# Kernel optimization log

Measured on AMD Instinct MI355X. Metric: run time of the kernel, lower is better.

The kernel has to match this reference:

```python
import jax, jax.numpy as jnp
import numpy as np
import math

NUM_HEADS = 16
D_MODEL = 1024
BATCH = 1
SEQ_LEN = 4096


def alibi_slopes(num_heads):
    # slopes m_h = (256 ** (1/H)) ** -(h+1)
    x = (2.0 ** 8) ** (1.0 / num_heads)
    return jnp.asarray([1.0 / x ** (i + 1) for i in range(num_heads)], dtype=jnp.float32)


def setup_inputs() -> dict:
    key = jax.random.key(0)
    k1, k2 = jax.random.split(key)
    x = jax.random.normal(k1, (BATCH, SEQ_LEN, D_MODEL), dtype=jnp.float32)
    # nn.Linear(d_model, 3*d_model, bias=False); store as [d_model, 3*d_model] so y = x @ w
    w_kqv = jax.random.normal(k2, (D_MODEL, 3 * D_MODEL), dtype=jnp.float32) * (1.0 / math.sqrt(D_MODEL))
    return {"x": x, "w_kqv": w_kqv}


def reference(x, w_kqv):
    B, S, D = x.shape
    H = NUM_HEADS
    dh = D // H
    scale = jnp.asarray(math.sqrt(D), dtype=x.dtype)  # module divides by sqrt(d_model)

    kqv = x @ w_kqv  # [B, S, 3D]
    # NOTE: original chunks as (key, query, value) in that order
    k, q, v = jnp.split(kqv, 3, axis=-1)
    q = q.reshape(B, S, H, dh)
    k = k.reshape(B, S, H, dh)
    v = v.reshape(B, S, H, dh)

    # ALiBi bias: m_h * (j - i), shape [H, S, S]
    pos = jnp.arange(S)
    rel = pos[None, :] - pos[:, None]  # [S, S], x - y
    slopes = alibi_slopes(H).astype(x.dtype)  # [H]
    bias = slopes[:, None, None] * rel.astype(x.dtype)  # [H, S, S]

    score = jnp.einsum('bihd,bjhd->bhij', q, k) / scale + bias[None]  # [B, H, S, S]
    causal = rel <= 0  # j <= i (lower triangular)
    score = jnp.where(causal[None, None], score, jnp.asarray(-jnp.inf, dtype=score.dtype))

    attn = jax.nn.softmax(score, axis=-1)
    out = jnp.einsum('bhij,bjhd->bihd', attn, v).reshape(B, S, D)
    return out
```

## Files before the change

kernel.cpp:

```cpp
#include <hip/hip_runtime.h>
#include <stdint.h>
#include <math.h>

#define SEQ 4096
#define DM  1024
#define NH  16
#define DH  64
#define LOG2E 1.44269504088896341f

typedef short bf16x8 __attribute__((ext_vector_type(8)));
typedef short bf16x4 __attribute__((ext_vector_type(4)));
typedef float f32x4  __attribute__((ext_vector_type(4)));
typedef uint32_t u32x4 __attribute__((ext_vector_type(4)));

typedef const __attribute__((address_space(1))) short* gptr_t;
typedef __attribute__((address_space(3))) short* lptr_t;

__device__ __forceinline__ short f2bf(float f) {
    union { float f; uint32_t u; } x; x.f = f;
    uint32_t r = (x.u + 0x7fffu + ((x.u >> 16) & 1u)) >> 16;
    return (short)r;
}
__device__ __forceinline__ short f2bf_trunc(float f) {
    union { float f; uint32_t u; } x; x.f = f;
    return (short)(x.u >> 16);
}
__device__ __forceinline__ uint32_t pkbf(float lo, float hi) {
    union { float f; uint32_t u; } a, b; a.f = lo; b.f = hi;
    return (a.u >> 16) | (b.u & 0xffff0000u);
}

__device__ __forceinline__ void load_lds16(const short* g, const short* l) {
    __builtin_amdgcn_global_load_lds((gptr_t)(uintptr_t)g,
                                     (lptr_t)(uint32_t)(uintptr_t)l, 16, 0, 0);
}

__global__ __launch_bounds__(256) void cvt_fused(const float* __restrict__ x,
                                                 const float* __restrict__ w,
                                                 short* __restrict__ xb,
                                                 short* __restrict__ wtb) {
    __shared__ float T[64][69];
    const int b = blockIdx.x;
    if (b < 2048) {
        const int i = (b * 256 + threadIdx.x) * 8;
        float4 a0 = ((const float4*)(x + i))[0];
        float4 a1 = ((const float4*)(x + i))[1];
        bf16x8 p;
        p[0]=f2bf(a0.x); p[1]=f2bf(a0.y); p[2]=f2bf(a0.z); p[3]=f2bf(a0.w);
        p[4]=f2bf(a1.x); p[5]=f2bf(a1.y); p[6]=f2bf(a1.z); p[7]=f2bf(a1.w);
        *(bf16x8*)(xb + i) = p;
        return;
    }
    const int bb = b - 2048;
    const int n0 = (bb % 48) * 64, k0 = (bb / 48) * 64;
    const int t = threadIdx.x;
    {
        const int kr = t >> 4, nc = (t & 15) * 4;
        #pragma unroll
        for (int i = 0; i < 4; ++i) {
            float4 v = *(const float4*)(w + (size_t)(k0 + kr + i * 16) * 3072 + n0 + nc);
            T[kr + i * 16][nc + 0] = v.x; T[kr + i * 16][nc + 1] = v.y;
            T[kr + i * 16][nc + 2] = v.z; T[kr + i * 16][nc + 3] = v.w;
        }
    }
    __syncthreads();
    const int nr = t >> 4, kc = (t & 15) * 4;
    #pragma unroll
    for (int i = 0; i < 4; ++i) {
        const int n = n0 + nr + i * 16;
        const float sc = (n >= 1024 && n < 2048) ? (LOG2E / 32.0f) : 1.0f;
        short4 o;
        o.x = f2bf(T[kc + 0][nr + i * 16] * sc);
        o.y = f2bf(T[kc + 1][nr + i * 16] * sc);
        o.z = f2bf(T[kc + 2][nr + i * 16] * sc);
        o.w = f2bf(T[kc + 3][nr + i * 16] * sc);
        *(short4*)(wtb + (size_t)n * 1024 + k0 + kc) = o;
    }
}

__global__ __launch_bounds__(256) void qkv_gemm(const short* __restrict__ xb,
                                                const short* __restrict__ wtb,
                                                short* __restrict__ kq,
                                                short* __restrict__ vt) {
    __shared__ short As[128 * 64];
    __shared__ short Bs[128 * 64];
    const int col0 = blockIdx.y * 128, row0 = blockIdx.x * 128;
    const int tid = threadIdx.x, w = tid >> 6, lane = tid & 63;
    const int lmod = lane & 15, ldiv = lane >> 4;
    const int wr = (w >> 1) * 64, wc = (w & 1) * 64;

    f32x4 acc[4][4] = {};
    const short* Ag = xb  + (size_t)row0 * DM;
    const short* Bg = wtb + (size_t)col0 * DM;

    for (int k0 = 0; k0 < DM; k0 += 64) {
        __syncthreads();
        #pragma unroll
        for (int t = 0; t < 4; ++t) {
            const int o = (w * 4 + t) * 1024 + lane * 16;
            const int r = o >> 7, cs = (o & 127) >> 1;
            load_lds16(Ag + (size_t)r * DM + k0 + cs, As + (w * 4 + t) * 512);
            load_lds16(Bg + (size_t)r * DM + k0 + cs, Bs + (w * 4 + t) * 512);
        }
        __syncthreads();
        #pragma unroll
        for (int ks = 0; ks < 2; ++ks) {
            bf16x8 af[4], bf[4];
            #pragma unroll
            for (int i = 0; i < 4; ++i)
                af[i] = *(const bf16x8*)(As + (wr + i * 16 + lmod) * 64 + ks * 32 + ldiv * 8);
            #pragma unroll
            for (int j = 0; j < 4; ++j)
                bf[j] = *(const bf16x8*)(Bs + (wc + j * 16 + lmod) * 64 + ks * 32 + ldiv * 8);
            #pragma unroll
            for (int i = 0; i < 4; ++i)
                #pragma unroll
                for (int j = 0; j < 4; ++j)
                    acc[i][j] = __builtin_amdgcn_mfma_f32_16x16x32_bf16(af[i], bf[j], acc[i][j], 0, 0, 0);
        }
    }

    if (col0 < 2048) {
        #pragma unroll
        for (int i = 0; i < 4; ++i)
            #pragma unroll
            for (int j = 0; j < 4; ++j)
                #pragma unroll
                for (int r = 0; r < 4; ++r)
                    kq[(size_t)(row0 + wr + i * 16 + ldiv * 4 + r) * 2048
                       + col0 + wc + j * 16 + lmod] = f2bf(acc[i][j][r]);
    } else {
        #pragma unroll
        for (int i = 0; i < 4; ++i) {
            const int ig = row0 + wr + i * 16 + ldiv * 4;
            const int kk = ig & 63;
            const int kkp = (kk & 32) | ((kk & 12) << 1) | ((kk & 16) >> 2);
            const int igp = (ig & ~63) | kkp;
            #pragma unroll
            for (int j = 0; j < 4; ++j) {
                const int cg = col0 + wc + j * 16 + lmod - 2048;
                const int h = cg >> 6, d = cg & 63;
                bf16x4 p;
                p[0]=f2bf(acc[i][j][0]); p[1]=f2bf(acc[i][j][1]);
                p[2]=f2bf(acc[i][j][2]); p[3]=f2bf(acc[i][j][3]);
                *(bf16x4*)(vt + (size_t)(h * 64 + d) * SEQ + igp) = p;
            }
        }
    }
}

__global__ __launch_bounds__(256, 4) void attn(const short* __restrict__ kq,
                                               const short* __restrict__ vt,
                                               float* __restrict__ o0,
                                               float* __restrict__ o1,
                                               float* __restrict__ ls0,
                                               float* __restrict__ ls1) {
    __shared__ short Ks[64 * 64];
    __shared__ short Vs[64 * 64];

    const int b = blockIdx.x;
    const int band = b >> 8, pos = b & 255, g = pos >> 5;
    const int qt = (band & 1) ? (24 - band * 8 + g) : (31 - band * 8 - g);
    const int h = (pos >> 1) & 15, s = pos & 1;

    const int tid = threadIdx.x, w = tid >> 6, lane = tid & 63;
    const int lmod = lane & 15, ldiv = lane >> 4;
    const float slope2 = exp2f(-0.5f * (float)(h + 1)) * LOG2E;

    const int sr0 = w * 16 + (lane >> 3), sr1 = sr0 + 8;
    const int sc0 = (lane & 7) ^ (sr0 & 7), sc1 = (lane & 7) ^ (sr1 & 7);

    const int xorm = lmod & 7;
    const int cxs0 = (ldiv ^ xorm) * 8;
    const int cxs1 = ((4 + ldiv) ^ xorm) * 8;

    const int rowbase = qt * 128 + w * 32;

    bf16x8 qf[2][2];
    #pragma unroll
    for (int m = 0; m < 2; ++m) {
        const short* qp = kq + (size_t)(rowbase + m * 16 + lmod) * 2048 + 1024 + h * 64;
        qf[m][0] = *(const bf16x8*)(qp + ldiv * 8);
        qf[m][1] = *(const bf16x8*)(qp + 32 + ldiv * 8);
    }
    int db2[2];
    float pre[2][4];
    #pragma unroll
    for (int m = 0; m < 2; ++m) {
        db2[m] = 4 * ldiv - (rowbase + m * 16 + lmod);
        #pragma unroll
        for (int r = 0; r < 4; ++r) pre[m][r] = slope2 * (float)(db2[m] + r);
    }

    f32x4 O[2][4] = {};
    float lsum[2] = {};
    const int kt0 = s ? (qt + 1) : 0;
    const int kt1 = s ? (2 * qt + 2) : (qt + 1);

    for (int kt = kt0; kt < kt1; ++kt) {
        __syncthreads();
        {
            const short* kb = kq + (size_t)(kt * 64) * 2048 + h * 64;
            load_lds16(kb + (size_t)sr0 * 2048 + sc0 * 8, Ks + (w * 16) * 64);
            load_lds16(kb + (size_t)sr1 * 2048 + sc1 * 8, Ks + (w * 16 + 8) * 64);
            const short* vb = vt + (size_t)(h * 64) * SEQ + kt * 64;
            load_lds16(vb + (size_t)sr0 * SEQ + sc0 * 8, Vs + (w * 16) * 64);
            load_lds16(vb + (size_t)sr1 * SEQ + sc1 * 8, Vs + (w * 16 + 8) * 64);
        }
        __syncthreads();

        const bool diag = (kt >= 2 * qt);
        const int dt = kt * 64;
        const float cb = slope2 * (float)dt;

        #pragma unroll
        for (int ks = 0; ks < 2; ++ks) {
            u32x4 pk0, pk1;
            #pragma unroll
            for (int j1 = 0; j1 < 2; ++j1) {
                const int nt = ks * 2 + j1;
                const float cn = cb + slope2 * (float)(nt * 16);
                f32x4 s0, s1;
                #pragma unroll
                for (int r = 0; r < 4; ++r) { s0[r] = pre[0][r] + cn; s1[r] = pre[1][r] + cn; }
                const short* krow = Ks + (nt * 16 + lmod) * 64;
                const bf16x8 kf0 = *(const bf16x8*)(krow + cxs0);
                const bf16x8 kf1 = *(const bf16x8*)(krow + cxs1);
                s0 = __builtin_amdgcn_mfma_f32_16x16x32_bf16(kf0, qf[0][0], s0, 0, 0, 0);
                s0 = __builtin_amdgcn_mfma_f32_16x16x32_bf16(kf1, qf[0][1], s0, 0, 0, 0);
                s1 = __builtin_amdgcn_mfma_f32_16x16x32_bf16(kf0, qf[1][0], s1, 0, 0, 0);
                s1 = __builtin_amdgcn_mfma_f32_16x16x32_bf16(kf1, qf[1][1], s1, 0, 0, 0);

                float p0[4], p1[4];
                if (diag) {
                    #pragma unroll
                    for (int r = 0; r < 4; ++r) {
                        float v0 = s0[r], v1 = s1[r];
                        if (dt + nt * 16 + r + db2[0] > 0) v0 = -1e30f;
                        if (dt + nt * 16 + r + db2[1] > 0) v1 = -1e30f;
                        p0[r] = __builtin_amdgcn_exp2f(v0);
                        p1[r] = __builtin_amdgcn_exp2f(v1);
                    }
                } else {
                    #pragma unroll
                    for (int r = 0; r < 4; ++r) {
                        p0[r] = __builtin_amdgcn_exp2f(s0[r]);
                        p1[r] = __builtin_amdgcn_exp2f(s1[r]);
                    }
                }
                lsum[0] += (p0[0] + p0[1]) + (p0[2] + p0[3]);
                lsum[1] += (p1[0] + p1[1]) + (p1[2] + p1[3]);
                pk0[j1 * 2]     = pkbf(p0[0], p0[1]);
                pk0[j1 * 2 + 1] = pkbf(p0[2], p0[3]);
                pk1[j1 * 2]     = pkbf(p1[0], p1[1]);
                pk1[j1 * 2 + 1] = pkbf(p1[2], p1[3]);
            }
            const bf16x8 pa0 = __builtin_bit_cast(bf16x8, pk0);
            const bf16x8 pa1 = __builtin_bit_cast(bf16x8, pk1);
            const int cxo = ks ? cxs1 : cxs0;
            #pragma unroll
            for (int nt2 = 0; nt2 < 4; ++nt2) {
                const bf16x8 vf = *(const bf16x8*)(Vs + (nt2 * 16 + lmod) * 64 + cxo);
                O[0][nt2] = __builtin_amdgcn_mfma_f32_16x16x32_bf16(pa0, vf, O[0][nt2], 0, 0, 0);
                O[1][nt2] = __builtin_amdgcn_mfma_f32_16x16x32_bf16(pa1, vf, O[1][nt2], 0, 0, 0);
            }
        }
    }

    #pragma unroll
    for (int m = 0; m < 2; ++m) {
        float v = lsum[m];
        v += __shfl_xor(v, 16);
        v += __shfl_xor(v, 32);
        lsum[m] = v;
    }

    float* ob = s ? o1 : o0;
    float* lb = s ? ls1 : ls0;
    #pragma unroll
    for (int m = 0; m < 2; ++m) {
        const int i0 = rowbase + m * 16 + ldiv * 4;
        #pragma unroll
        for (int nt2 = 0; nt2 < 4; ++nt2)
            #pragma unroll
            for (int r = 0; r < 4; ++r)
                ob[(size_t)(i0 + r) * DM + h * 64 + nt2 * 16 + lmod] = O[m][nt2][r];
    }
    if (ldiv == 0) {
        #pragma unroll
        for (int m = 0; m < 2; ++m)
            lb[h * SEQ + rowbase + m * 16 + lmod] = lsum[m];
    }
}

__global__ __launch_bounds__(256) void combine(float* __restrict__ out,
                                               const float* __restrict__ opart,
                                               const float* __restrict__ ls0,
                                               const float* __restrict__ ls1) {
    const int i8 = (blockIdx.x * 256 + threadIdx.x) * 8;
    const int row = i8 >> 10, col = i8 & 1023, h = col >> 6;
    const float l = ls0[h * SEQ + row] + ls1[h * SEQ + row];
    const float rc = 1.0f / l;
    float4 a0 = *(const float4*)(out + i8);
    float4 a1 = *(const float4*)(out + i8 + 4);
    float4 b0 = *(const float4*)(opart + i8);
    float4 b1 = *(const float4*)(opart + i8 + 4);
    float4 c0, c1;
    c0.x = (a0.x + b0.x) * rc; c0.y = (a0.y + b0.y) * rc;
    c0.z = (a0.z + b0.z) * rc; c0.w = (a0.w + b0.w) * rc;
    c1.x = (a1.x + b1.x) * rc; c1.y = (a1.y + b1.y) * rc;
    c1.z = (a1.z + b1.z) * rc; c1.w = (a1.w + b1.w) * rc;
    *(float4*)(out + i8) = c0;
    *(float4*)(out + i8 + 4) = c1;
}

extern "C" void kernel_launch(void* const* d_in, const int* in_sizes, int n_in,
                              void* d_out, int out_size, void* d_ws, size_t ws_size,
                              hipStream_t stream) {
    const float* x = (const float*)d_in[0];
    const float* w = (const float*)d_in[1];
    float* out = (float*)d_out;

    char* ws = (char*)d_ws;
    short* kq    = (short*)(ws);
    short* vt    = (short*)(ws + ((size_t)16 << 20));
    short* xb    = (short*)(ws + ((size_t)24 << 20));
    short* wtb   = (short*)(ws + ((size_t)32 << 20));
    float* opart = (float*)(ws + ((size_t)24 << 20));
    float* ls0   = (float*)(ws + ((size_t)40 << 20));
    float* ls1   = (float*)(ws + ((size_t)40 << 20) + (256 << 10));

    cvt_fused<<<2048 + 768, 256, 0, stream>>>(x, w, xb, wtb);
    qkv_gemm <<<dim3(SEQ / 128, 3072 / 128), 256, 0, stream>>>(xb, wtb, kq, vt);
    attn     <<<1024, 256, 0, stream>>>(kq, vt, out, opart, ls0, ls1);
    combine  <<<SEQ * DM / (256 * 8), 256, 0, stream>>>(out, opart, ls0, ls1);
}
```

Baseline: 181.9 us.

## Double-buffer QKV GEMM LDS tiles with swizzled layout and manual waitcnt scheduling

Rewrites the QKV projection GEMM main loop to use two LDS buffers. The next k-tile's global-to-LDS loads are issued while MFMAs run on the current tile, using explicit vmcnt/lgkmcnt waits and raw s_barrier. The LDS layout now uses an XOR swizzle on 16-byte columns to avoid bank conflicts on ds_read_b128. It also requests two workgroups per CU. Together these aim to hide global load latency and LDS stalls. In exchange it doubles LDS use per block and depends on hand-counted wait values being correct.

```diff
diff --git a/kernel.cpp b/kernel.cpp
--- a/kernel.cpp
+++ b/kernel.cpp
@@ -21,10 +21,6 @@
     uint32_t r = (x.u + 0x7fffu + ((x.u >> 16) & 1u)) >> 16;
     return (short)r;
 }
-__device__ __forceinline__ short f2bf_trunc(float f) {
-    union { float f; uint32_t u; } x; x.f = f;
-    return (short)(x.u >> 16);
-}
 __device__ __forceinline__ uint32_t pkbf(float lo, float hi) {
     union { float f; uint32_t u; } a, b; a.f = lo; b.f = hi;
     return (a.u >> 16) | (b.u & 0xffff0000u);
@@ -34,6 +30,14 @@
     __builtin_amdgcn_global_load_lds((gptr_t)(uintptr_t)g,
                                      (lptr_t)(uint32_t)(uintptr_t)l, 16, 0, 0);
 }
+
+__device__ __forceinline__ void wgbar() {
+    asm volatile("" ::: "memory");
+    __builtin_amdgcn_s_barrier();
+    asm volatile("" ::: "memory");
+}
+#define WAITVM(n) asm volatile("s_waitcnt vmcnt(" #n ")" ::: "memory")
+#define DSR(d, a, o) asm volatile("ds_read_b128 %0, %1 offset:" o : "=v"(d) : "v"(a))
 
 __global__ __launch_bounds__(256) void cvt_fused(const float* __restrict__ x,
                                                  const float* __restrict__ w,
@@ -78,45 +82,85 @@
     }
 }
 
-__global__ __launch_bounds__(256) void qkv_gemm(const short* __restrict__ xb,
-                                                const short* __restrict__ wtb,
-                                                short* __restrict__ kq,
-                                                short* __restrict__ vt) {
-    __shared__ short As[128 * 64];
-    __shared__ short Bs[128 * 64];
+__global__ __launch_bounds__(256, 2) void qkv_gemm(const short* __restrict__ xb,
+                                                   const short* __restrict__ wtb,
+                                                   short* __restrict__ kq,
+                                                   short* __restrict__ vt) {
+    __shared__ short As[2][8192];
+    __shared__ short Bs[2][8192];
     const int col0 = blockIdx.y * 128, row0 = blockIdx.x * 128;
     const int tid = threadIdx.x, w = tid >> 6, lane = tid & 63;
     const int lmod = lane & 15, ldiv = lane >> 4;
     const int wr = (w >> 1) * 64, wc = (w & 1) * 64;
 
+    const int srow = w * 32 + (lane >> 3);
+    const int slc  = (lane & 7) ^ ((lane >> 3) & 7);
+    const short* gA = xb  + (size_t)(row0 + srow) * 1024 + slc * 8;
+    const short* gB = wtb + (size_t)(col0 + srow) * 1024 + slc * 8;
+    short* lA = &As[0][0] + w * 2048;
+    short* lB = &Bs[0][0] + w * 2048;
+
+    const uint32_t asb = (uint32_t)(uintptr_t)&As[0][0];
+    const uint32_t bsb = (uint32_t)(uintptr_t)&Bs[0][0];
+    const int xorm = lmod & 7;
+    const int rdA = (wr + lmod) * 128 + ((ldiv ^ xorm) << 4);
+    const int rdB = (wc + lmod) * 128 + ((ldiv ^ xorm) << 4);
+
     f32x4 acc[4][4] = {};
-    const short* Ag = xb  + (size_t)row0 * DM;
-    const short* Bg = wtb + (size_t)col0 * DM;
-
-    for (int k0 = 0; k0 < DM; k0 += 64) {
-        __syncthreads();
-        #pragma unroll
-        for (int t = 0; t < 4; ++t) {
-            const int o = (w * 4 + t) * 1024 + lane * 16;
-            const int r = o >> 7, cs = (o & 127) >> 1;
-            load_lds16(Ag + (size_t)r * DM + k0 + cs, As + (w * 4 + t) * 512);
-            load_lds16(Bg + (size_t)r * DM + k0 + cs, Bs + (w * 4 + t) * 512);
-        }
-        __syncthreads();
-        #pragma unroll
-        for (int ks = 0; ks < 2; ++ks) {
-            bf16x8 af[4], bf[4];
-            #pragma unroll
-            for (int i = 0; i < 4; ++i)
-                af[i] = *(const bf16x8*)(As + (wr + i * 16 + lmod) * 64 + ks * 32 + ldiv * 8);
+
+    auto stage = [&](int kt, int p) {
+        const short* ga = gA + kt * 64;
+        const short* gb = gB + kt * 64;
+        short* la = lA + p * 8192;
+        short* lb = lB + p * 8192;
+        #pragma unroll
+        for (int q = 0; q < 4; ++q) {
+            load_lds16(ga + q * 8192, la + q * 512);
+            load_lds16(gb + q * 8192, lb + q * 512);
+        }
+    };
+
+    stage(0, 0);
+    stage(1, 1);
+    WAITVM(8);
+    wgbar();
+
+    for (int t = 0; t < 16; ++t) {
+        const int poff = (t & 1) << 14;
+        const int aA0 = (int)asb + poff + rdA, aA1 = aA0 ^ 64;
+        const int bA0 = (int)bsb + poff + rdB, bA1 = bA0 ^ 64;
+        bf16x8 a0[4], a1[4], b0[4], b1[4];
+        DSR(a0[0], aA0, "0");    DSR(a0[1], aA0, "2048");
+        DSR(a0[2], aA0, "4096"); DSR(a0[3], aA0, "6144");
+        DSR(b0[0], bA0, "0");    DSR(b0[1], bA0, "2048");
+        DSR(b0[2], bA0, "4096"); DSR(b0[3], bA0, "6144");
+        DSR(a1[0], aA1, "0");    DSR(a1[1], aA1, "2048");
+        DSR(a1[2], aA1, "4096"); DSR(a1[3], aA1, "6144");
+        DSR(b1[0], bA1, "0");    DSR(b1[1], bA1, "2048");
+        DSR(b1[2], bA1, "4096"); DSR(b1[3], bA1, "6144");
+        asm volatile("s_waitcnt lgkmcnt(8)" ::: "memory");
+        __builtin_amdgcn_sched_barrier(0);
+        #pragma unroll
+        for (int i = 0; i < 4; ++i)
             #pragma unroll
             for (int j = 0; j < 4; ++j)
-                bf[j] = *(const bf16x8*)(Bs + (wc + j * 16 + lmod) * 64 + ks * 32 + ldiv * 8);
-            #pragma unroll
-            for (int i = 0; i < 4; ++i)
-                #pragma unroll
-                for (int j = 0; j < 4; ++j)
-                    acc[i][j] = __builtin_amdgcn_mfma_f32_16x16x32_bf16(af[i], bf[j], acc[i][j], 0, 0, 0);
+                acc[i][j] = __builtin_amdgcn_mfma_f32_16x16x32_bf16(a0[i], b0[j], acc[i][j], 0, 0, 0);
+        asm volatile("s_waitcnt lgkmcnt(0)" ::: "memory");
+        __builtin_amdgcn_sched_barrier(0);
+        #pragma unroll
+        for (int i = 0; i < 4; ++i)
+            #pragma unroll
+            for (int j = 0; j < 4; ++j)
+                acc[i][j] = __builtin_amdgcn_mfma_f32_16x16x32_bf16(a1[i], b1[j], acc[i][j], 0, 0, 0);
+
+        wgbar();
+        if (t + 2 < 16) {
+            stage(t + 2, t & 1);
+            WAITVM(8);
+            wgbar();
+        } else if (t + 1 < 16) {
+            WAITVM(0);
+            wgbar();
         }
     }
 
```

New measurement: 160.3 us. 11.9% less time.
